# Kernel tuning notes

Measured on AMD Instinct MI355X. Metric: run time of the kernel, lower is better.

## Reference

```python
import jax, jax.numpy as jnp
import numpy as np

POWERS = (0, 1, 2)
IN_F, OUT_F = 64, 64
B, N, T = 8, 2048, 12


def setup_inputs() -> dict:
    key = jax.random.key(0)
    ks = jax.random.split(key, 8)
    inp = {
        "x": jax.random.normal(ks[0], (B, IN_F, N, T), dtype=jnp.float32),
        "adj": jax.random.uniform(ks[1], (B, N, N), dtype=jnp.float32),
    }
    # Xavier-uniform weights per adjacency power, zero biases (as in initialize_weights)
    limit = float(np.sqrt(6.0 / (IN_F + OUT_F)))
    for i, p in enumerate(POWERS):
        inp[f"W{p}"] = jax.random.uniform(ks[2 + i], (IN_F, OUT_F), jnp.float32, -limit, limit)
        inp[f"b{p}"] = jnp.zeros((OUT_F,), jnp.float32)
    return inp


def _gcn_conv(x, adj, W, b, a_power):
    # x: [B, F, N, T]; W: [F, O]; adj: [B, N, N]
    h = jnp.einsum('bfnt,fo->bont', x, W) + b[None, :, None, None]
    # repeated diffusion along node axis: h[f, n] <- sum_m adj[n, m] h[f, m]
    for _ in range(a_power):
        h = jnp.einsum('bnm,bomt->bont', adj, h)
    return jax.nn.leaky_relu(h)  # default negative_slope 0.01, same as torch


def reference(x, adj, W0, b0, W1, b1, W2, b2):
    params = {0: (W0, b0), 1: (W1, b1), 2: (W2, b2)}
    outs = [_gcn_conv(x, adj, params[p][0], params[p][1], p) for p in POWERS]
    return jnp.concatenate(outs, axis=1)  # [B, len(POWERS)*O, N, T]
```

## Files before the change

kernel.cpp:

```cpp
#include <hip/hip_runtime.h>

#define B_ 8
#define N_ 2048
#define T_ 12
#define F_ 64
#define NT 24576
#define CH 192
#define C_ 768

typedef __bf16 bf16x8 __attribute__((ext_vector_type(8)));
typedef float f32x4 __attribute__((ext_vector_type(4)));
typedef float f32x16 __attribute__((ext_vector_type(16)));

typedef const __attribute__((address_space(1))) unsigned int as1_uint;
typedef __attribute__((address_space(3))) unsigned int as3_uint;

__device__ __forceinline__ void gload16(const void* g, void* l) {
  __builtin_amdgcn_global_load_lds((as1_uint*)g, (as3_uint*)l, 16, 0, 0);
}

__device__ __forceinline__ unsigned short f2bf(float f) {
  unsigned int u = __float_as_uint(f);
  u += 0x7FFFu + ((u >> 16) & 1u);
  return (unsigned short)(u >> 16);
}

__device__ __forceinline__ float bf2f(unsigned short u) {
  return __uint_as_float(((unsigned int)u) << 16);
}

__device__ __forceinline__ float leaky(float v) {
  return v >= 0.0f ? v : 0.01f * v;
}

__global__ __launch_bounds__(256) void convert_rs_k(const float* __restrict__ adj,
                                                    unsigned short* __restrict__ adjb,
                                                    float* __restrict__ rs1) {
  const int row = blockIdx.x;
  const int tid = threadIdx.x;
  const int lane = tid & 63;
  const int wave = tid >> 6;
  const float4* src = reinterpret_cast<const float4*>(adj + (size_t)row * N_);
  ushort4* dst = reinterpret_cast<ushort4*>(adjb + (size_t)row * N_);

  float s = 0.0f;
#pragma unroll
  for (int i = tid; i < 512; i += 256) {
    const float4 v = src[i];
    ushort4 u;
    u.x = f2bf(v.x); u.y = f2bf(v.y); u.z = f2bf(v.z); u.w = f2bf(v.w);
    dst[i] = u;
    s += v.x + v.y + v.z + v.w;
  }
#pragma unroll
  for (int o = 32; o; o >>= 1) s += __shfl_xor(s, o);
  __shared__ float red[4];
  if (lane == 0) red[wave] = s;
  __syncthreads();
  if (tid == 0) rs1[row] = red[0] + red[1] + red[2] + red[3];
}

__global__ __launch_bounds__(256) void rs2_k(const unsigned short* __restrict__ adjb,
                                             const float* __restrict__ rs1,
                                             float* __restrict__ rs2) {
  const int row = blockIdx.x;
  const int b = row >> 11;
  const int tid = threadIdx.x;
  const int lane = tid & 63;
  const int wave = tid >> 6;
  const ushort4* src = reinterpret_cast<const ushort4*>(adjb + (size_t)row * N_);
  const float* r1 = rs1 + ((size_t)b << 11);

  float s = 0.0f;
#pragma unroll
  for (int i = tid; i < 512; i += 256) {
    const ushort4 a = src[i];
    const int m = i * 4;
    s += bf2f(a.x) * r1[m] + bf2f(a.y) * r1[m + 1]
       + bf2f(a.z) * r1[m + 2] + bf2f(a.w) * r1[m + 3];
  }
#pragma unroll
  for (int o = 32; o; o >>= 1) s += __shfl_xor(s, o);
  __shared__ float red[4];
  if (lane == 0) red[wave] = s;
  __syncthreads();
  if (tid == 0) rs2[row] = red[0] + red[1] + red[2] + red[3];
}

__global__ __launch_bounds__(256) void convertX_k(const float* __restrict__ x,
                                                  unsigned short* __restrict__ Xt) {
  __shared__ float xl[T_][260];
  const int tid = threadIdx.x;
  const int n0 = blockIdx.x * 256;
  const int f = blockIdx.y;
  const int b = blockIdx.z;

  const float* src = x + (((size_t)b * F_ + f) * N_ + n0 + tid) * T_;
  float4 v0 = *reinterpret_cast<const float4*>(src);
  float4 v1 = *reinterpret_cast<const float4*>(src + 4);
  float4 v2 = *reinterpret_cast<const float4*>(src + 8);
  xl[0][tid] = v0.x;  xl[1][tid] = v0.y;  xl[2][tid] = v0.z;  xl[3][tid] = v0.w;
  xl[4][tid] = v1.x;  xl[5][tid] = v1.y;  xl[6][tid] = v1.z;  xl[7][tid] = v1.w;
  xl[8][tid] = v2.x;  xl[9][tid] = v2.y;  xl[10][tid] = v2.z; xl[11][tid] = v2.w;
  __syncthreads();
#pragma unroll
  for (int t = 0; t < T_; ++t)
    Xt[((size_t)b * C_ + f * T_ + t) * N_ + n0 + tid] = f2bf(xl[t][tid]);
}

__device__ __forceinline__ void stage_wt(const float* __restrict__ W,
                                         unsigned short* Wt, int tid) {
  const int f = tid >> 2;
  const int q = tid & 3;
  const float4* row = reinterpret_cast<const float4*>(W + f * 64 + q * 16);
#pragma unroll
  for (int v4 = 0; v4 < 4; ++v4) {
    float4 v = row[v4];
    const int ob = q * 16 + v4 * 4;
    Wt[(ob + 0) * 72 + f] = f2bf(v.x);
    Wt[(ob + 1) * 72 + f] = f2bf(v.y);
    Wt[(ob + 2) * 72 + f] = f2bf(v.z);
    Wt[(ob + 3) * 72 + f] = f2bf(v.w);
  }
}

__global__ __launch_bounds__(256) void p0_k(const float* __restrict__ x,
                                            const float* __restrict__ W0,
                                            const float* __restrict__ bia0,
                                            float* __restrict__ out) {
  __shared__ unsigned short Wt[64 * 72];
  __shared__ float bias[64];
  const int tid = threadIdx.x;
  stage_wt(W0, Wt, tid);
  if (tid < 64) bias[tid] = bia0[tid];
  __syncthreads();

  const int lane = tid & 63;
  const int wave = tid >> 6;
  const int b = blockIdx.y;
  const int e = blockIdx.x * 64 + wave * 16 + (lane & 15);
  const int fgrp = (lane >> 4) * 8;
  const float* xb = x + (size_t)b * F_ * NT;

  bf16x8 xf[2];
#pragma unroll
  for (int kf = 0; kf < 2; ++kf)
#pragma unroll
    for (int j = 0; j < 8; ++j)
      xf[kf][j] = (__bf16)xb[(size_t)(fgrp + kf * 32 + j) * NT + e];

  float* outb = out + (size_t)b * CH * NT;
#pragma unroll
  for (int ob = 0; ob < 4; ++ob) {
    f32x4 acc = {};
#pragma unroll
    for (int kf = 0; kf < 2; ++kf) {
      bf16x8 af = *reinterpret_cast<const bf16x8*>(
          &Wt[(ob * 16 + (lane & 15)) * 72 + kf * 32 + fgrp]);
      acc = __builtin_amdgcn_mfma_f32_16x16x32_bf16(af, xf[kf], acc, 0, 0, 0);
    }
#pragma unroll
    for (int r = 0; r < 4; ++r) {
      const int o = ob * 16 + (lane >> 4) * 4 + r;
      outb[(size_t)o * NT + e] = leaky(acc[r] + bias[o]);
    }
  }
}

__global__ __launch_bounds__(256) void pT_k(const unsigned short* __restrict__ Yt,
                                            const float* __restrict__ W,
                                            const float* __restrict__ bia,
                                            const float* __restrict__ rs,
                                            float* __restrict__ out,
                                            const int ocb) {
  __shared__ unsigned short Wt[64 * 72];
  __shared__ float bias[64];
  const int tid = threadIdx.x;
  stage_wt(W, Wt, tid);
  if (tid < 64) bias[tid] = bia[tid];
  __syncthreads();

  const int lane = tid & 63;
  const int wave = tid >> 6;
  const int b = blockIdx.y;
  const int n = blockIdx.x * 16 + (lane & 15);
  const int fgrp = (lane >> 4) * 8;
  const __bf16* Yb = reinterpret_cast<const __bf16*>(Yt + (size_t)b * C_ * N_);
  const float rsv = rs[((size_t)b << 11) + n];
  float* outb = out + (size_t)b * CH * NT;

#pragma unroll
  for (int it = 0; it < 3; ++it) {
    const int t = wave * 3 + it;

    bf16x8 xf[2];
#pragma unroll
    for (int kf = 0; kf < 2; ++kf)
#pragma unroll
      for (int j = 0; j < 8; ++j)
        xf[kf][j] = Yb[(size_t)((kf * 32 + fgrp + j) * T_ + t) * N_ + n];

#pragma unroll
    for (int ob = 0; ob < 4; ++ob) {
      f32x4 acc = {};
#pragma unroll
      for (int kf = 0; kf < 2; ++kf) {
        bf16x8 af = *reinterpret_cast<const bf16x8*>(
            &Wt[(ob * 16 + (lane & 15)) * 72 + kf * 32 + fgrp]);
        acc = __builtin_amdgcn_mfma_f32_16x16x32_bf16(af, xf[kf], acc, 0, 0, 0);
      }
#pragma unroll
      for (int r = 0; r < 4; ++r) {
        const int o = ob * 16 + (lane >> 4) * 4 + r;
        outb[(size_t)(ocb + o) * NT + n * T_ + t] = leaky(acc[r] + rsv * bias[o]);
      }
    }
  }
}

__global__ __launch_bounds__(256, 2) void gemmB_k(
    const unsigned short* __restrict__ adjb,
    const unsigned short* __restrict__ Bt,
    unsigned short* __restrict__ Ht)
{
  __shared__ __align__(16) unsigned short lds[20480];

  const int tid  = threadIdx.x;
  const int lane = tid & 63;
  const int wave = tid >> 6;
  const int wm = wave >> 1;
  const int wn = wave & 1;

  const int b  = blockIdx.x & 7;
  const int j  = blockIdx.x >> 3;
  const int n0 = (j & 15) * 128;
  const int c0 = (j >> 4) * 192;

  const unsigned short* A  = adjb + (size_t)b * N_ * N_;
  const unsigned short* Bm = Bt   + (size_t)b * C_ * N_;

  const int swz = ((lane & 7) ^ (lane >> 3)) * 8;
  const unsigned short* aSt = A + (size_t)(n0 + wave * 32 + (lane >> 3)) * N_ + swz;
  const unsigned short* bSt = Bm + (size_t)(c0 + wave * 48 + (lane >> 3)) * N_ + swz;

  const int l31 = lane & 31;
  const int x7  = lane & 7;
  const int hi  = lane >> 5;
  const int sh  = (lane >> 1) & 3;
  const int e0  = hi ^ (x7 & 1);
  const int aBase0 = (wm * 64 + l31) * 64;
  const int bBase0 = 8192 + (wn * 96 + l31) * 64;

  f32x16 acc[2][3] = {};

#define STG(KT) \
  gload16(aSt + (KT) * 64,            lds + wave * 2048); \
  gload16(aSt + 8 * N_ + (KT) * 64,   lds + wave * 2048 + 512); \
  gload16(aSt + 16 * N_ + (KT) * 64,  lds + wave * 2048 + 1024); \
  gload16(aSt + 24 * N_ + (KT) * 64,  lds + wave * 2048 + 1536); \
  gload16(bSt + (KT) * 64,            lds + 8192 + wave * 3072); \
  gload16(bSt + 8 * N_ + (KT) * 64,   lds + 8192 + wave * 3072 + 512); \
  gload16(bSt + 16 * N_ + (KT) * 64,  lds + 8192 + wave * 3072 + 1024); \
  gload16(bSt + 24 * N_ + (KT) * 64,  lds + 8192 + wave * 3072 + 1536); \
  gload16(bSt + 32 * N_ + (KT) * 64,  lds + 8192 + wave * 3072 + 2048); \
  gload16(bSt + 40 * N_ + (KT) * 64,  lds + 8192 + wave * 3072 + 2560);

  STG(0)

#pragma unroll 1
  for (int kt = 0; kt < 32; ++kt) {
    __syncthreads();
#pragma unroll
    for (int s = 0; s < 4; ++s) {
      const int ge = ((((s) ^ sh) << 1) | e0) * 8;
      bf16x8 af[2], bfv[3];
#pragma unroll
      for (int m = 0; m < 2; ++m)
        af[m] = *(const bf16x8*)(lds + aBase0 + m * 2048 + ge);
#pragma unroll
      for (int nf = 0; nf < 3; ++nf)
        bfv[nf] = *(const bf16x8*)(lds + bBase0 + nf * 2048 + ge);
#pragma unroll
      for (int m = 0; m < 2; ++m)
#pragma unroll
        for (int nf = 0; nf < 3; ++nf)
          acc[m][nf] = __builtin_amdgcn_mfma_f32_32x32x16_bf16(
              af[m], bfv[nf], acc[m][nf], 0, 0, 0);
    }
    __syncthreads();
    if (kt + 1 < 32) { STG(kt + 1) }
  }

  unsigned short* Hb = Ht + (size_t)b * C_ * N_;
#pragma unroll
  for (int m = 0; m < 2; ++m) {
#pragma unroll
    for (int nf = 0; nf < 3; ++nf) {
      const int c = c0 + wn * 96 + nf * 32 + l31;
#pragma unroll
      for (int q = 0; q < 4; ++q) {
        const int nb = n0 + wm * 64 + m * 32 + q * 8 + 4 * hi;
        ushort4 u;
        u.x = f2bf(acc[m][nf][q * 4 + 0]);
        u.y = f2bf(acc[m][nf][q * 4 + 1]);
        u.z = f2bf(acc[m][nf][q * 4 + 2]);
        u.w = f2bf(acc[m][nf][q * 4 + 3]);
        *reinterpret_cast<ushort4*>(&Hb[(size_t)c * N_ + nb]) = u;
      }
    }
  }
#undef STG
}

extern "C" void kernel_launch(void* const* d_in, const int* in_sizes, int n_in,
                              void* d_out, int out_size, void* d_ws, size_t ws_size,
                              hipStream_t stream) {
  const float* x   = (const float*)d_in[0];
  const float* adj = (const float*)d_in[1];
  const float* W0  = (const float*)d_in[2];
  const float* b0  = (const float*)d_in[3];
  const float* W1  = (const float*)d_in[4];
  const float* b1  = (const float*)d_in[5];
  const float* W2  = (const float*)d_in[6];
  const float* b2  = (const float*)d_in[7];
  float* out = (float*)d_out;

  char* ws = (char*)d_ws;
  unsigned short* adjb = (unsigned short*)ws;
  unsigned short* R1   = (unsigned short*)(ws + 67108864);
  unsigned short* R2   = (unsigned short*)(ws + 92274688);
  float* rs1 = (float*)(ws + 117440512);
  float* rs2 = (float*)(ws + 117506048);

  hipLaunchKernelGGL(convert_rs_k, dim3(B_ * N_), dim3(256), 0, stream,
                     adj, adjb, rs1);

  hipLaunchKernelGGL(convertX_k, dim3(N_ / 256, F_, B_), dim3(256), 0, stream,
                     x, R1);

  hipLaunchKernelGGL(p0_k, dim3(NT / 64, B_), dim3(256), 0, stream,
                     x, W0, b0, out);

  hipLaunchKernelGGL(gemmB_k, dim3(512), dim3(256), 0, stream,
                     adjb, R1, R2);

  hipLaunchKernelGGL(rs2_k, dim3(B_ * N_), dim3(256), 0, stream,
                     adjb, rs1, rs2);

  hipLaunchKernelGGL(pT_k, dim3(N_ / 16, B_), dim3(256), 0, stream,
                     R2, W1, b1, rs1, out, 64);

  hipLaunchKernelGGL(gemmB_k, dim3(512), dim3(256), 0, stream,
                     adjb, R2, R1);

  hipLaunchKernelGGL(pT_k, dim3(N_ / 16, B_), dim3(256), 0, stream,
                     R1, W2, b2, rs2, out, 128);
}
```

Baseline: 266.9 us.

## Pre-swizzle adjacency into MFMA fragment layout and stream A directly from global

The bf16 adjacency is now written in a fragment-major layout: each 32-row by 16-column tile is stored as one contiguous 64-lane block. The GEMM can then load A operands straight from global/L2 into registers with a single 16-byte load per lane, instead of staging A through LDS. Only B is staged in LDS, now double-buffered so the next tile's loads are issued before the current MFMAs, with one barrier per k-step instead of two. Occupancy is raised to 3 blocks per CU. The risk is that the direct global A loads sit on the MFMA critical path with no LDS reuse across the two N-waves that share them, and the row-sum kernels are rewritten to match the new layout.

Result: slower. 300.9 us (+12.7%).

```diff
diff --git a/kernel.cpp b/kernel.cpp
--- a/kernel.cpp
+++ b/kernel.cpp
@@ -33,58 +33,69 @@
   return v >= 0.0f ? v : 0.01f * v;
 }
 
-__global__ __launch_bounds__(256) void convert_rs_k(const float* __restrict__ adj,
-                                                    unsigned short* __restrict__ adjb,
-                                                    float* __restrict__ rs1) {
-  const int row = blockIdx.x;
-  const int tid = threadIdx.x;
-  const int lane = tid & 63;
-  const int wave = tid >> 6;
-  const float4* src = reinterpret_cast<const float4*>(adj + (size_t)row * N_);
-  ushort4* dst = reinterpret_cast<ushort4*>(adjb + (size_t)row * N_);
-
-  float s = 0.0f;
-#pragma unroll
-  for (int i = tid; i < 512; i += 256) {
-    const float4 v = src[i];
-    ushort4 u;
-    u.x = f2bf(v.x); u.y = f2bf(v.y); u.z = f2bf(v.z); u.w = f2bf(v.w);
-    dst[i] = u;
-    s += v.x + v.y + v.z + v.w;
-  }
-#pragma unroll
-  for (int o = 32; o; o >>= 1) s += __shfl_xor(s, o);
-  __shared__ float red[4];
-  if (lane == 0) red[wave] = s;
-  __syncthreads();
-  if (tid == 0) rs1[row] = red[0] + red[1] + red[2] + red[3];
-}
-
-__global__ __launch_bounds__(256) void rs2_k(const unsigned short* __restrict__ adjb,
+__global__ __launch_bounds__(256) void convertAf_k(const float* __restrict__ adj,
+                                                   unsigned short* __restrict__ Af,
+                                                   float* __restrict__ rs1) {
+  const int tid = threadIdx.x;
+  const int lane = tid & 63;
+  const int wave = tid >> 6;
+  const int ng = blockIdx.x;
+  const int b  = blockIdx.y;
+  const int row = ng * 32 + (lane & 31);
+
+  const float* srcRow = adj + ((size_t)b * N_ + row) * N_ + (lane >> 5) * 8;
+  unsigned short* dstB = Af + ((size_t)(b * 64 + ng) * 128) * 512 + lane * 8;
+
+  float rsum = 0.0f;
+#pragma unroll 4
+  for (int kg = wave; kg < 128; kg += 4) {
+    const float* s = srcRow + kg * 16;
+    const float4 v0 = *reinterpret_cast<const float4*>(s);
+    const float4 v1 = *reinterpret_cast<const float4*>(s + 4);
+    rsum += v0.x + v0.y + v0.z + v0.w + v1.x + v1.y + v1.z + v1.w;
+    ushort4 a, c;
+    a.x = f2bf(v0.x); a.y = f2bf(v0.y); a.z = f2bf(v0.z); a.w = f2bf(v0.w);
+    c.x = f2bf(v1.x); c.y = f2bf(v1.y); c.z = f2bf(v1.z); c.w = f2bf(v1.w);
+    unsigned short* d = dstB + (size_t)kg * 512;
+    *reinterpret_cast<ushort4*>(d) = a;
+    *reinterpret_cast<ushort4*>(d + 4) = c;
+  }
+  rsum += __shfl_xor(rsum, 32);
+  __shared__ float red[4][32];
+  if (lane < 32) red[wave][lane] = rsum;
+  __syncthreads();
+  if (tid < 32)
+    rs1[((size_t)b << 11) + ng * 32 + tid] =
+        red[0][tid] + red[1][tid] + red[2][tid] + red[3][tid];
+}
+
+__global__ __launch_bounds__(256) void rs2_k(const unsigned short* __restrict__ Af,
                                              const float* __restrict__ rs1,
                                              float* __restrict__ rs2) {
-  const int row = blockIdx.x;
-  const int b = row >> 11;
-  const int tid = threadIdx.x;
-  const int lane = tid & 63;
-  const int wave = tid >> 6;
-  const ushort4* src = reinterpret_cast<const ushort4*>(adjb + (size_t)row * N_);
-  const float* r1 = rs1 + ((size_t)b << 11);
+  const int tid = threadIdx.x;
+  const int lane = tid & 63;
+  const int wave = tid >> 6;
+  const int ng = blockIdx.x;
+  const int b  = blockIdx.y;
+
+  const unsigned short* srcB = Af + ((size_t)(b * 64 + ng) * 128) * 512 + lane * 8;
+  const float* r1b = rs1 + ((size_t)b << 11) + (lane >> 5) * 8;
 
   float s = 0.0f;
-#pragma unroll
-  for (int i = tid; i < 512; i += 256) {
-    const ushort4 a = src[i];
-    const int m = i * 4;
-    s += bf2f(a.x) * r1[m] + bf2f(a.y) * r1[m + 1]
-       + bf2f(a.z) * r1[m + 2] + bf2f(a.w) * r1[m + 3];
-  }
-#pragma unroll
-  for (int o = 32; o; o >>= 1) s += __shfl_xor(s, o);
-  __shared__ float red[4];
-  if (lane == 0) red[wave] = s;
-  __syncthreads();
-  if (tid == 0) rs2[row] = red[0] + red[1] + red[2] + red[3];
+#pragma unroll 4
+  for (int kg = wave; kg < 128; kg += 4) {
+    const bf16x8 a = *reinterpret_cast<const bf16x8*>(srcB + (size_t)kg * 512);
+    const float* r1 = r1b + kg * 16;
+#pragma unroll
+    for (int j = 0; j < 8; ++j) s += (float)a[j] * r1[j];
+  }
+  s += __shfl_xor(s, 32);
+  __shared__ float red[4][32];
+  if (lane < 32) red[wave][lane] = s;
+  __syncthreads();
+  if (tid < 32)
+    rs2[((size_t)b << 11) + ng * 32 + tid] =
+        red[0][tid] + red[1][tid] + red[2][tid] + red[3][tid];
 }
 
 __global__ __launch_bounds__(256) void convertX_k(const float* __restrict__ x,
@@ -218,12 +229,12 @@
   }
 }
 
-__global__ __launch_bounds__(256, 2) void gemmB_k(
-    const unsigned short* __restrict__ adjb,
+__global__ __launch_bounds__(256, 3) void gemmS_k(
+    const unsigned short* __restrict__ Af,
     const unsigned short* __restrict__ Bt,
     unsigned short* __restrict__ Ht)
 {
-  __shared__ __align__(16) unsigned short lds[20480];
+  __shared__ __align__(16) unsigned short lds[2][12288];
 
   const int tid  = threadIdx.x;
   const int lane = tid & 63;
@@ -236,59 +247,57 @@
   const int n0 = (j & 15) * 128;
   const int c0 = (j >> 4) * 192;
 
-  const unsigned short* A  = adjb + (size_t)b * N_ * N_;
-  const unsigned short* Bm = Bt   + (size_t)b * C_ * N_;
+  const unsigned short* Bm = Bt + (size_t)b * C_ * N_;
+
+  const unsigned short* aP0 =
+      Af + ((size_t)(b * 64 + (n0 >> 5) + wm * 2 + 0) * 128) * 512 + lane * 8;
+  const unsigned short* aP1 =
+      Af + ((size_t)(b * 64 + (n0 >> 5) + wm * 2 + 1) * 128) * 512 + lane * 8;
 
   const int swz = ((lane & 7) ^ (lane >> 3)) * 8;
-  const unsigned short* aSt = A + (size_t)(n0 + wave * 32 + (lane >> 3)) * N_ + swz;
   const unsigned short* bSt = Bm + (size_t)(c0 + wave * 48 + (lane >> 3)) * N_ + swz;
+  const int ldsW = wave * 3072;
 
   const int l31 = lane & 31;
   const int x7  = lane & 7;
   const int hi  = lane >> 5;
   const int sh  = (lane >> 1) & 3;
   const int e0  = hi ^ (x7 & 1);
-  const int aBase0 = (wm * 64 + l31) * 64;
-  const int bBase0 = 8192 + (wn * 96 + l31) * 64;
+  const int bBase = (wn * 96 + l31) * 64;
 
   f32x16 acc[2][3] = {};
 
-#define STG(KT) \
-  gload16(aSt + (KT) * 64,            lds + wave * 2048); \
-  gload16(aSt + 8 * N_ + (KT) * 64,   lds + wave * 2048 + 512); \
-  gload16(aSt + 16 * N_ + (KT) * 64,  lds + wave * 2048 + 1024); \
-  gload16(aSt + 24 * N_ + (KT) * 64,  lds + wave * 2048 + 1536); \
-  gload16(bSt + (KT) * 64,            lds + 8192 + wave * 3072); \
-  gload16(bSt + 8 * N_ + (KT) * 64,   lds + 8192 + wave * 3072 + 512); \
-  gload16(bSt + 16 * N_ + (KT) * 64,  lds + 8192 + wave * 3072 + 1024); \
-  gload16(bSt + 24 * N_ + (KT) * 64,  lds + 8192 + wave * 3072 + 1536); \
-  gload16(bSt + 32 * N_ + (KT) * 64,  lds + 8192 + wave * 3072 + 2048); \
-  gload16(bSt + 40 * N_ + (KT) * 64,  lds + 8192 + wave * 3072 + 2560);
-
-  STG(0)
+#define STG(S, KT) \
+  gload16(bSt + (KT) * 64,            lds[S] + ldsW); \
+  gload16(bSt + 8 * N_ + (KT) * 64,   lds[S] + ldsW + 512); \
+  gload16(bSt + 16 * N_ + (KT) * 64,  lds[S] + ldsW + 1024); \
+  gload16(bSt + 24 * N_ + (KT) * 64,  lds[S] + ldsW + 1536); \
+  gload16(bSt + 32 * N_ + (KT) * 64,  lds[S] + ldsW + 2048); \
+  gload16(bSt + 40 * N_ + (KT) * 64,  lds[S] + ldsW + 2560);
+
+  STG(0, 0)
 
 #pragma unroll 1
   for (int kt = 0; kt < 32; ++kt) {
     __syncthreads();
+    const int S = kt & 1;
+    if (kt + 1 < 32) { STG((kt + 1) & 1, kt + 1) }
 #pragma unroll
     for (int s = 0; s < 4; ++s) {
-      const int ge = ((((s) ^ sh) << 1) | e0) * 8;
-      bf16x8 af[2], bfv[3];
-#pragma unroll
-      for (int m = 0; m < 2; ++m)
-        af[m] = *(const bf16x8*)(lds + aBase0 + m * 2048 + ge);
-#pragma unroll
-      for (int nf = 0; nf < 3; ++nf)
-        bfv[nf] = *(const bf16x8*)(lds + bBase0 + nf * 2048 + ge);
-#pragma unroll
-      for (int m = 0; m < 2; ++m)
-#pragma unroll
-        for (int nf = 0; nf < 3; ++nf)
-          acc[m][nf] = __builtin_amdgcn_mfma_f32_32x32x16_bf16(
-              af[m], bfv[nf], acc[m][nf], 0, 0, 0);
-    }
-    __syncthreads();
-    if (kt + 1 < 32) { STG(kt + 1) }
+      const size_t kg = (size_t)(kt * 4 + s) * 512;
+      bf16x8 af0 = *reinterpret_cast<const bf16x8*>(aP0 + kg);
+      bf16x8 af1 = *reinterpret_cast<const bf16x8*>(aP1 + kg);
+      const int ge = (((s ^ sh) << 1) | e0) * 8;
+      bf16x8 bv0 = *(const bf16x8*)(lds[S] + bBase + 0 * 2048 + ge);
+      bf16x8 bv1 = *(const bf16x8*)(lds[S] + bBase + 1 * 2048 + ge);
+      bf16x8 bv2 = *(const bf16x8*)(lds[S] + bBase + 2 * 2048 + ge);
+      acc[0][0] = __builtin_amdgcn_mfma_f32_32x32x16_bf16(af0, bv0, acc[0][0], 0, 0, 0);
+      acc[0][1] = __builtin_amdgcn_mfma_f32_32x32x16_bf16(af0, bv1, acc[0][1], 0, 0, 0);
+      acc[0][2] = __builtin_amdgcn_mfma_f32_32x32x16_bf16(af0, bv2, acc[0][2], 0, 0, 0);
+      acc[1][0] = __builtin_amdgcn_mfma_f32_32x32x16_bf16(af1, bv0, acc[1][0], 0, 0, 0);
+      acc[1][1] = __builtin_amdgcn_mfma_f32_32x32x16_bf16(af1, bv1, acc[1][1], 0, 0, 0);
+      acc[1][2] = __builtin_amdgcn_mfma_f32_32x32x16_bf16(af1, bv2, acc[1][2], 0, 0, 0);
+    }
   }
 
   unsigned short* Hb = Ht + (size_t)b * C_ * N_;
@@ -326,14 +335,14 @@
   float* out = (float*)d_out;
 
   char* ws = (char*)d_ws;
-  unsigned short* adjb = (unsigned short*)ws;
-  unsigned short* R1   = (unsigned short*)(ws + 67108864);
-  unsigned short* R2   = (unsigned short*)(ws + 92274688);
+  unsigned short* Af = (unsigned short*)ws;
+  unsigned short* R1 = (unsigned short*)(ws + 67108864);
+  unsigned short* R2 = (unsigned short*)(ws + 92274688);
   float* rs1 = (float*)(ws + 117440512);
   float* rs2 = (float*)(ws + 117506048);
 
-  hipLaunchKernelGGL(convert_rs_k, dim3(B_ * N_), dim3(256), 0, stream,
-                     adj, adjb, rs1);
+  hipLaunchKernelGGL(convertAf_k, dim3(64, 8), dim3(256), 0, stream,
+                     adj, Af, rs1);
 
   hipLaunchKernelGGL(convertX_k, dim3(N_ / 256, F_, B_), dim3(256), 0, stream,
                      x, R1);
@@ -341,17 +350,17 @@
   hipLaunchKernelGGL(p0_k, dim3(NT / 64, B_), dim3(256), 0, stream,
                      x, W0, b0, out);
 
-  hipLaunchKernelGGL(gemmB_k, dim3(512), dim3(256), 0, stream,
-                     adjb, R1, R2);
-
-  hipLaunchKernelGGL(rs2_k, dim3(B_ * N_), dim3(256), 0, stream,
-                     adjb, rs1, rs2);
+  hipLaunchKernelGGL(gemmS_k, dim3(512), dim3(256), 0, stream,
+                     Af, R1, R2);
+
+  hipLaunchKernelGGL(rs2_k, dim3(64, 8), dim3(256), 0, stream,
+                     Af, rs1, rs2);
 
   hipLaunchKernelGGL(pT_k, dim3(N_ / 16, B_), dim3(256), 0, stream,
                      R2, W1, b1, rs1, out, 64);
 
-  hipLaunchKernelGGL(gemmB_k, dim3(512), dim3(256), 0, stream,
-                     adjb, R2, R1);
+  hipLaunchKernelGGL(gemmS_k, dim3(512), dim3(256), 0, stream,
+                     Af, R2, R1);
 
   hipLaunchKernelGGL(pT_k, dim3(N_ / 16, B_), dim3(256), 0, stream,
                      R1, W2, b2, rs2, out, 128);
```
